# Kernel optimization log

Hardware: AMD Instinct MI355X
Metric: run time of the kernel (lower is better)

The kernel has to match this reference:

```python
import jax, jax.numpy as jnp
import numpy as np

N = 100000      # number of 1-simplices (edges of the power grid)
NNZ = 3200000   # nonzeros in L1_tilde (avg degree 32)
CIN = 128
COUT = 128
BN_EPS = 1e-5


def setup_inputs() -> dict:
    key = jax.random.key(0)
    ks = jax.random.split(key, 8)
    Z_H = jax.random.normal(ks[0], (N, CIN), dtype=jnp.float32)
    rows = jax.random.randint(ks[1], (NNZ,), 0, N)
    cols = jax.random.randint(ks[2], (NNZ,), 0, N)
    values = jax.random.normal(ks[3], (NNZ,), dtype=jnp.float32)
    # nn.Linear params (Kaiming-ish scale)
    W = jax.random.normal(ks[4], (CIN, COUT), dtype=jnp.float32) / np.float32(np.sqrt(CIN))
    b = jnp.zeros((COUT,), dtype=jnp.float32)
    # BatchNorm1d affine params
    gamma = jnp.ones((COUT,), dtype=jnp.float32)
    beta = jnp.zeros((COUT,), dtype=jnp.float32)
    return {"Z_H": Z_H, "values": values, "W": W, "b": b,
            "gamma": gamma, "beta": beta, "rows": rows, "cols": cols}


def reference(Z_H, values, W, b, gamma, beta, rows, cols):
    # Linear projection: [N, CIN] @ [CIN, COUT] + [COUT]
    Z_theta = Z_H @ W + b
    # Sparse Laplacian matmul (COO SpMM): Z_conv[r] += v * Z_theta[c]
    gathered = values[:, None] * Z_theta[cols]          # [NNZ, COUT]
    Z_conv = jax.ops.segment_sum(gathered, rows, num_segments=Z_H.shape[0])
    # BatchNorm1d (training mode: biased batch stats over the node dim)
    mean = jnp.mean(Z_conv, axis=0)
    var = jnp.var(Z_conv, axis=0)
    Z_bn = (Z_conv - mean) * (gamma / jnp.sqrt(var + BN_EPS)) + beta
    # ReLU + row-wise max pool -> [N, 1]
    Z_psi = jax.nn.relu(Z_bn)
    return jnp.max(Z_psi, axis=1, keepdims=True)
```

## Files before the change

kernel.cpp:

```cpp
#include <hip/hip_runtime.h>
#include <hip/hip_bf16.h>

#define CIN  128
#define COUT 128
#define BN_EPS 1e-5f
#define RPB   256
#define MAXNB 512
#define PCHUNK 8192
#define CAP   10240

typedef __attribute__((ext_vector_type(8))) short short8;
typedef __attribute__((ext_vector_type(4))) float f32x4;

__device__ __forceinline__ unsigned short f2bf(float f) {
    unsigned u = __float_as_uint(f);
    u += 0x7fffu + ((u >> 16) & 1u);
    return (unsigned short)(u >> 16);
}

__global__ __launch_bounds__(256, 2) void gemm_mfma_kernel(
    const float* __restrict__ Z, const float* __restrict__ W,
    const float* __restrict__ b, unsigned short* __restrict__ Zt, int N)
{
    const int lane = threadIdx.x & 63;
    const int wid  = threadIdx.x >> 6;
    const int lm   = lane & 15;
    const int lg   = lane >> 4;

    short8 bfr[4][8];
#pragma unroll
    for (int kc = 0; kc < 4; ++kc) {
#pragma unroll
        for (int ct = 0; ct < 8; ++ct) {
            union { short8 v; unsigned short u[8]; } bf;
#pragma unroll
            for (int e = 0; e < 8; ++e)
                bf.u[e] = f2bf(W[(kc * 32 + lg * 8 + e) * COUT + ct * 16 + lm]);
            bfr[kc][ct] = bf.v;
        }
    }

    float bias[8];
#pragma unroll
    for (int ct = 0; ct < 8; ++ct) bias[ct] = b[ct * 16 + lm];

    const int ntiles = (N + 63) / 64;
    for (int tile = blockIdx.x; tile < ntiles; tile += gridDim.x) {
        const int row0 = tile * 64 + wid * 16;
        if (row0 >= N) continue;

        const int arow = row0 + lm;
        const bool aval = arow < N;
        const float* zrow = Z + (size_t)arow * CIN;

        f32x4 acc[8];
#pragma unroll
        for (int ct = 0; ct < 8; ++ct) {
            f32x4 a = {bias[ct], bias[ct], bias[ct], bias[ct]};
            acc[ct] = a;
        }

#pragma unroll
        for (int kc = 0; kc < 4; ++kc) {
            union { short8 v; unsigned short u[8]; } af;
            if (aval) {
                const float4 z0 = *((const float4*)(zrow + kc * 32 + lg * 8));
                const float4 z1 = *((const float4*)(zrow + kc * 32 + lg * 8 + 4));
                af.u[0] = f2bf(z0.x); af.u[1] = f2bf(z0.y);
                af.u[2] = f2bf(z0.z); af.u[3] = f2bf(z0.w);
                af.u[4] = f2bf(z1.x); af.u[5] = f2bf(z1.y);
                af.u[6] = f2bf(z1.z); af.u[7] = f2bf(z1.w);
            } else {
#pragma unroll
                for (int e = 0; e < 8; ++e) af.u[e] = 0;
            }
#pragma unroll
            for (int ct = 0; ct < 8; ++ct)
                acc[ct] = __builtin_amdgcn_mfma_f32_16x16x32_bf16(
                    af.v, bfr[kc][ct], acc[ct], 0, 0, 0);
        }

#pragma unroll
        for (int i = 0; i < 4; ++i) {
            const int grow = row0 + lg * 4 + i;
            if (grow < N) {
#pragma unroll
                for (int ct = 0; ct < 8; ++ct)
                    Zt[(size_t)grow * COUT + ct * 16 + lm] = f2bf(acc[ct][i]);
            }
        }
    }
}

__global__ __launch_bounds__(256) void partition_kernel(
    const int* __restrict__ rows, const int* __restrict__ cols,
    const float* __restrict__ vals, int* __restrict__ bucketCur,
    uint2* __restrict__ ebuck, int nnz, int NB)
{
    __shared__ int h[MAXNB];
    __shared__ int basecur[MAXNB];
    const int t = threadIdx.x;

    for (int i = t; i < NB; i += 256) h[i] = 0;
    __syncthreads();

    const int c0 = blockIdx.x * PCHUNK;
    const int ce = min(c0 + PCHUNK, nnz);

    int rloc[PCHUNK / 256];
#pragma unroll
    for (int j = 0; j < PCHUNK / 256; ++j) {
        const int i = c0 + j * 256 + t;
        int r = -1;
        if (i < ce) r = rows[i];
        rloc[j] = r;
        if (r >= 0) atomicAdd(&h[r >> 8], 1);
    }
    __syncthreads();

    for (int i = t; i < NB; i += 256) {
        const int c = h[i];
        basecur[i] = c ? (i * CAP + atomicAdd(&bucketCur[i], c)) : 0;
    }
    __syncthreads();

#pragma unroll
    for (int j = 0; j < PCHUNK / 256; ++j) {
        const int i = c0 + j * 256 + t;
        const int r = rloc[j];
        if (r >= 0) {
            const int p = atomicAdd(&basecur[r >> 8], 1);
            ebuck[p] = make_uint2((unsigned)cols[i] | ((unsigned)(r & (RPB - 1)) << 17),
                                  __float_as_uint(vals[i]));
        }
    }
}

__global__ __launch_bounds__(1024) void bucket_build_kernel(
    const uint2* __restrict__ ebuck, const int* __restrict__ bucketCur,
    uint2* __restrict__ epack, uint2* __restrict__ rowinfo, int N)
{
    __shared__ int cnt[RPB];
    __shared__ int sc[RPB];
    __shared__ int loc[RPB];

    const int b    = blockIdx.x;
    const int base = b * CAP;
    const int count = bucketCur[b];
    const int t = threadIdx.x;

    if (t < RPB) cnt[t] = 0;
    __syncthreads();

    for (int i = t; i < count; i += 1024)
        atomicAdd(&cnt[ebuck[base + i].x >> 17], 1);
    __syncthreads();

    if (t < RPB) sc[t] = cnt[t];
    __syncthreads();
#pragma unroll
    for (int off = 1; off < RPB; off <<= 1) {
        int v = 0;
        if (t < RPB && t >= off) v = sc[t - off];
        __syncthreads();
        if (t < RPB) sc[t] += v;
        __syncthreads();
    }

    if (t < RPB) {
        const int start = sc[t] - cnt[t];
        loc[t] = start;
        const int row = b * RPB + t;
        if (row < N) rowinfo[row] = make_uint2((unsigned)(base + start), (unsigned)cnt[t]);
    }
    __syncthreads();

    for (int i = t; i < count; i += 1024) {
        const uint2 e = ebuck[base + i];
        const int rl  = (int)(e.x >> 17);
        const int pos = atomicAdd(&loc[rl], 1);
        epack[base + pos] = make_uint2(e.x & 0x1FFFFu, e.y);
    }
}

__global__ __launch_bounds__(256) void gather_kernel(
    const unsigned short* __restrict__ Zt, const uint2* __restrict__ epack,
    const uint2* __restrict__ rowinfo, unsigned int* __restrict__ Zc,
    float* __restrict__ stats, int N)
{
    __shared__ float sbuf[256];
    sbuf[threadIdx.x] = 0.f;
    __syncthreads();

    const int wid  = threadIdx.x >> 6;
    const int lane = threadIdx.x & 63;
    const int eo   = lane >> 5;
    const int cg   = lane & 31;

    float s0 = 0.f, s1 = 0.f, s2 = 0.f, s3 = 0.f;
    float q0 = 0.f, q1 = 0.f, q2 = 0.f, q3 = 0.f;

    for (int row = blockIdx.x * 4 + wid; row < N; row += gridDim.x * 4) {
        const uint2 ri = rowinfo[row];
        const int beg = (int)ri.x;
        const int end = beg + (int)ri.y;

        float a0 = 0.f, a1 = 0.f, a2 = 0.f, a3 = 0.f;

        int i = beg + eo;
        for (; i + 6 < end; i += 8) {
            const uint2 p0 = epack[i];
            const uint2 p1 = epack[i + 2];
            const uint2 p2 = epack[i + 4];
            const uint2 p3 = epack[i + 6];
            const uint2 g0 = *((const uint2*)(Zt + (size_t)p0.x * COUT + cg * 4));
            const uint2 g1 = *((const uint2*)(Zt + (size_t)p1.x * COUT + cg * 4));
            const uint2 g2 = *((const uint2*)(Zt + (size_t)p2.x * COUT + cg * 4));
            const uint2 g3 = *((const uint2*)(Zt + (size_t)p3.x * COUT + cg * 4));
            const float v0 = __uint_as_float(p0.y);
            const float v1 = __uint_as_float(p1.y);
            const float v2 = __uint_as_float(p2.y);
            const float v3 = __uint_as_float(p3.y);
            a0 = fmaf(v0, __uint_as_float(g0.x << 16), a0);
            a1 = fmaf(v0, __uint_as_float(g0.x & 0xffff0000u), a1);
            a2 = fmaf(v0, __uint_as_float(g0.y << 16), a2);
            a3 = fmaf(v0, __uint_as_float(g0.y & 0xffff0000u), a3);
            a0 = fmaf(v1, __uint_as_float(g1.x << 16), a0);
            a1 = fmaf(v1, __uint_as_float(g1.x & 0xffff0000u), a1);
            a2 = fmaf(v1, __uint_as_float(g1.y << 16), a2);
            a3 = fmaf(v1, __uint_as_float(g1.y & 0xffff0000u), a3);
            a0 = fmaf(v2, __uint_as_float(g2.x << 16), a0);
            a1 = fmaf(v2, __uint_as_float(g2.x & 0xffff0000u), a1);
            a2 = fmaf(v2, __uint_as_float(g2.y << 16), a2);
            a3 = fmaf(v2, __uint_as_float(g2.y & 0xffff0000u), a3);
            a0 = fmaf(v3, __uint_as_float(g3.x << 16), a0);
            a1 = fmaf(v3, __uint_as_float(g3.x & 0xffff0000u), a1);
            a2 = fmaf(v3, __uint_as_float(g3.y << 16), a2);
            a3 = fmaf(v3, __uint_as_float(g3.y & 0xffff0000u), a3);
        }
        for (; i < end; i += 2) {
            const uint2 p = epack[i];
            const uint2 g = *((const uint2*)(Zt + (size_t)p.x * COUT + cg * 4));
            const float vp = __uint_as_float(p.y);
            a0 = fmaf(vp, __uint_as_float(g.x << 16), a0);
            a1 = fmaf(vp, __uint_as_float(g.x & 0xffff0000u), a1);
            a2 = fmaf(vp, __uint_as_float(g.y << 16), a2);
            a3 = fmaf(vp, __uint_as_float(g.y & 0xffff0000u), a3);
        }

        a0 += __shfl_xor(a0, 32);
        a1 += __shfl_xor(a1, 32);
        a2 += __shfl_xor(a2, 32);
        a3 += __shfl_xor(a3, 32);

        if (eo == 0) {
            uint2 o;
            o.x = (unsigned)f2bf(a0) | ((unsigned)f2bf(a1) << 16);
            o.y = (unsigned)f2bf(a2) | ((unsigned)f2bf(a3) << 16);
            *((uint2*)(Zc + (size_t)row * (COUT / 2) + cg * 2)) = o;
            s0 += a0; s1 += a1; s2 += a2; s3 += a3;
            q0 = fmaf(a0, a0, q0);
            q1 = fmaf(a1, a1, q1);
            q2 = fmaf(a2, a2, q2);
            q3 = fmaf(a3, a3, q3);
        }
    }

    if (eo == 0) {
        const int c0 = cg * 4;
        atomicAdd(&sbuf[c0 + 0], s0);
        atomicAdd(&sbuf[c0 + 1], s1);
        atomicAdd(&sbuf[c0 + 2], s2);
        atomicAdd(&sbuf[c0 + 3], s3);
        atomicAdd(&sbuf[128 + c0 + 0], q0);
        atomicAdd(&sbuf[128 + c0 + 1], q1);
        atomicAdd(&sbuf[128 + c0 + 2], q2);
        atomicAdd(&sbuf[128 + c0 + 3], q3);
    }
    __syncthreads();
    atomicAdd(&stats[threadIdx.x], sbuf[threadIdx.x]);
}

__global__ __launch_bounds__(256) void finalize_kernel(
    const unsigned int* __restrict__ Zc, const float* __restrict__ stats,
    const float* __restrict__ gamma, const float* __restrict__ beta,
    float* __restrict__ out, int N)
{
    const int row = blockIdx.x * 4 + (threadIdx.x >> 6);
    if (row >= N) return;
    const int lane = threadIdx.x & 63;
    const int c0 = lane * 2;

    const unsigned g = Zc[(size_t)row * (COUT / 2) + lane];
    const float x0 = __uint_as_float(g << 16);
    const float x1 = __uint_as_float(g & 0xffff0000u);

    const float invN = 1.0f / (float)N;
    const float m0 = stats[c0] * invN;
    const float m1 = stats[c0 + 1] * invN;
    const float v0 = stats[128 + c0] * invN - m0 * m0;
    const float v1 = stats[128 + c0 + 1] * invN - m1 * m1;
    const float sc0 = gamma[c0]     * rsqrtf(v0 + BN_EPS);
    const float sc1 = gamma[c0 + 1] * rsqrtf(v1 + BN_EPS);

    float y0 = (x0 - m0) * sc0 + beta[c0];
    float y1 = (x1 - m1) * sc1 + beta[c0 + 1];
    y0 = fmaxf(y0, 0.f);
    y1 = fmaxf(y1, 0.f);

    float mx = fmaxf(y0, y1);
#pragma unroll
    for (int off = 32; off > 0; off >>= 1)
        mx = fmaxf(mx, __shfl_xor(mx, off));

    if (lane == 0) out[row] = mx;
}

extern "C" void kernel_launch(void* const* d_in, const int* in_sizes, int n_in,
                              void* d_out, int out_size, void* d_ws, size_t ws_size,
                              hipStream_t stream)
{
    const float* Z_H   = (const float*)d_in[0];
    const float* vals  = (const float*)d_in[1];
    const float* W     = (const float*)d_in[2];
    const float* b     = (const float*)d_in[3];
    const float* gamma = (const float*)d_in[4];
    const float* beta  = (const float*)d_in[5];
    const int*   rows  = (const int*)d_in[6];
    const int*   cols  = (const int*)d_in[7];
    float* out = (float*)d_out;

    const int N   = in_sizes[0] / CIN;
    const int nnz = in_sizes[1];
    const int NB  = (N + RPB - 1) / RPB;
    const int pblocks = (nnz + PCHUNK - 1) / PCHUNK;

    char* ws = (char*)d_ws;
    size_t off = 0;
    unsigned short* Zt = (unsigned short*)(ws + off); off += (size_t)N * COUT * sizeof(unsigned short);
    unsigned int*   Zc = (unsigned int*)(ws + off);   off += (size_t)N * (COUT / 2) * sizeof(unsigned int);
    uint2* ebuck  = (uint2*)(ws + off);  off += (size_t)NB * CAP * sizeof(uint2);
    uint2* epack  = (uint2*)(ws + off);  off += (size_t)NB * CAP * sizeof(uint2);
    uint2* rowinfo = (uint2*)(ws + off); off += (size_t)N * sizeof(uint2);
    int* bucketCur = (int*)(ws + off);   off += (size_t)NB * sizeof(int);
    float* stats   = (float*)(ws + off); off += 256 * sizeof(float);

    hipMemsetAsync(bucketCur, 0, ((size_t)NB + 256) * sizeof(int), stream);

    gemm_mfma_kernel<<<512, 256, 0, stream>>>(Z_H, W, b, Zt, N);

    partition_kernel<<<pblocks, 256, 0, stream>>>(
        rows, cols, vals, bucketCur, ebuck, nnz, NB);
    bucket_build_kernel<<<NB, 1024, 0, stream>>>(ebuck, bucketCur, epack, rowinfo, N);

    gather_kernel<<<2048, 256, 0, stream>>>(Zt, epack, rowinfo, Zc, stats, N);

    finalize_kernel<<<(N + 3) / 4, 256, 0, stream>>>(Zc, stats, gamma, beta, out, N);
}
```

Before: 278.9 us.

## Fuse GEMM and edge partition into one launch; shrink row buckets to 64

The MFMA projection and the COO partition pass now run as one kernel, with the first 512 blocks doing GEMM tiles and the rest partitioning edges, so the two independent stages overlap and one launch is dropped. Buckets shrink from 256 to 64 rows with smaller capacity, and the bucket build uses 256-thread blocks, giving more, smaller blocks. Side effects: more buckets for the partition histogram (2048 shared slots), a tighter per-bucket capacity that could overflow on skewed inputs, and partition blocks now share the GEMM's launch bounds.

Result: faster. 271.8 us (-2.5%).

```diff
diff --git a/kernel.cpp b/kernel.cpp
--- a/kernel.cpp
+++ b/kernel.cpp
@@ -4,10 +4,11 @@
 #define CIN  128
 #define COUT 128
 #define BN_EPS 1e-5f
-#define RPB   256
-#define MAXNB 512
+#define RPB   64
+#define MAXNB 2048
 #define PCHUNK 8192
-#define CAP   10240
+#define CAP   2560
+#define GB    512
 
 typedef __attribute__((ext_vector_type(8))) short short8;
 typedef __attribute__((ext_vector_type(4))) float f32x4;
@@ -18,9 +19,10 @@
     return (unsigned short)(u >> 16);
 }
 
-__global__ __launch_bounds__(256, 2) void gemm_mfma_kernel(
+__device__ __forceinline__ void gemm_body(
     const float* __restrict__ Z, const float* __restrict__ W,
-    const float* __restrict__ b, unsigned short* __restrict__ Zt, int N)
+    const float* __restrict__ b, unsigned short* __restrict__ Zt,
+    int N, int bid)
 {
     const int lane = threadIdx.x & 63;
     const int wid  = threadIdx.x >> 6;
@@ -45,7 +47,7 @@
     for (int ct = 0; ct < 8; ++ct) bias[ct] = b[ct * 16 + lm];
 
     const int ntiles = (N + 63) / 64;
-    for (int tile = blockIdx.x; tile < ntiles; tile += gridDim.x) {
+    for (int tile = bid; tile < ntiles; tile += GB) {
         const int row0 = tile * 64 + wid * 16;
         if (row0 >= N) continue;
 
@@ -92,10 +94,10 @@
     }
 }
 
-__global__ __launch_bounds__(256) void partition_kernel(
+__device__ __forceinline__ void partition_body(
     const int* __restrict__ rows, const int* __restrict__ cols,
     const float* __restrict__ vals, int* __restrict__ bucketCur,
-    uint2* __restrict__ ebuck, int nnz, int NB)
+    uint2* __restrict__ ebuck, int nnz, int NB, int pb)
 {
     __shared__ int h[MAXNB];
     __shared__ int basecur[MAXNB];
@@ -104,7 +106,7 @@
     for (int i = t; i < NB; i += 256) h[i] = 0;
     __syncthreads();
 
-    const int c0 = blockIdx.x * PCHUNK;
+    const int c0 = pb * PCHUNK;
     const int ce = min(c0 + PCHUNK, nnz);
 
     int rloc[PCHUNK / 256];
@@ -114,7 +116,7 @@
         int r = -1;
         if (i < ce) r = rows[i];
         rloc[j] = r;
-        if (r >= 0) atomicAdd(&h[r >> 8], 1);
+        if (r >= 0) atomicAdd(&h[r >> 6], 1);
     }
     __syncthreads();
 
@@ -129,14 +131,28 @@
         const int i = c0 + j * 256 + t;
         const int r = rloc[j];
         if (r >= 0) {
-            const int p = atomicAdd(&basecur[r >> 8], 1);
+            const int p = atomicAdd(&basecur[r >> 6], 1);
             ebuck[p] = make_uint2((unsigned)cols[i] | ((unsigned)(r & (RPB - 1)) << 17),
                                   __float_as_uint(vals[i]));
         }
     }
 }
 
-__global__ __launch_bounds__(1024) void bucket_build_kernel(
+__global__ __launch_bounds__(256, 2) void gemm_part_kernel(
+    const float* __restrict__ Z, const float* __restrict__ W,
+    const float* __restrict__ b, unsigned short* __restrict__ Zt,
+    const int* __restrict__ rows, const int* __restrict__ cols,
+    const float* __restrict__ vals, int* __restrict__ bucketCur,
+    uint2* __restrict__ ebuck, int nnz, int N, int NB)
+{
+    if (blockIdx.x < GB) {
+        gemm_body(Z, W, b, Zt, N, blockIdx.x);
+    } else {
+        partition_body(rows, cols, vals, bucketCur, ebuck, nnz, NB, blockIdx.x - GB);
+    }
+}
+
+__global__ __launch_bounds__(256) void bucket_build_kernel(
     const uint2* __restrict__ ebuck, const int* __restrict__ bucketCur,
     uint2* __restrict__ epack, uint2* __restrict__ rowinfo, int N)
 {
@@ -152,7 +168,7 @@
     if (t < RPB) cnt[t] = 0;
     __syncthreads();
 
-    for (int i = t; i < count; i += 1024)
+    for (int i = t; i < count; i += 256)
         atomicAdd(&cnt[ebuck[base + i].x >> 17], 1);
     __syncthreads();
 
@@ -175,7 +191,7 @@
     }
     __syncthreads();
 
-    for (int i = t; i < count; i += 1024) {
+    for (int i = t; i < count; i += 256) {
         const uint2 e = ebuck[base + i];
         const int rl  = (int)(e.x >> 17);
         const int pos = atomicAdd(&loc[rl], 1);
@@ -347,11 +363,10 @@
 
     hipMemsetAsync(bucketCur, 0, ((size_t)NB + 256) * sizeof(int), stream);
 
-    gemm_mfma_kernel<<<512, 256, 0, stream>>>(Z_H, W, b, Zt, N);
-
-    partition_kernel<<<pblocks, 256, 0, stream>>>(
-        rows, cols, vals, bucketCur, ebuck, nnz, NB);
-    bucket_build_kernel<<<NB, 1024, 0, stream>>>(ebuck, bucketCur, epack, rowinfo, N);
+    gemm_part_kernel<<<GB + pblocks, 256, 0, stream>>>(
+        Z_H, W, b, Zt, rows, cols, vals, bucketCur, ebuck, nnz, N, NB);
+
+    bucket_build_kernel<<<NB, 256, 0, stream>>>(ebuck, bucketCur, epack, rowinfo, N);
 
     gather_kernel<<<2048, 256, 0, stream>>>(Zt, epack, rowinfo, Zc, stats, N);
 
```
